# Optimization experiments

Hardware: AMD Instinct MI355X
Metric: run time of the kernel (lower is better)

The kernel has to match this reference:

```python
import jax, jax.numpy as jnp
import numpy as np

OUT, IN, GROUP, BITS = 8192, 8192, 128, 4
NG = IN // GROUP  # 64 groups per row

def unpack4(qweight):
    # qweight: [OUT, IN//2] uint8 -> [OUT, IN] int, low nibble first
    low = qweight & jnp.uint8(0x0F)
    high = qweight >> jnp.uint8(4)
    return jnp.stack([low, high], axis=-1).reshape(qweight.shape[0], -1)

def dequantize(qw, scale, zero):
    # qw: [OUT, IN] ints; scale/zero: [OUT, NG]
    q = qw.astype(scale.dtype).reshape(OUT, NG, GROUP)
    w = (q - zero[:, :, None]) * scale[:, :, None]
    return w.reshape(OUT, IN)

def setup_inputs() -> dict:
    key = jax.random.key(0)
    k1, k2, k3, k4 = jax.random.split(key, 4)
    x = jax.random.normal(k1, (8, IN), dtype=jnp.float32)
    qweight = jax.random.randint(k2, (OUT, IN // 2), 0, 256, dtype=jnp.int32).astype(jnp.uint8)
    scale = (jax.random.uniform(k3, (OUT, NG), dtype=jnp.float32) * 0.02 + 0.001)
    zero = jax.random.uniform(k4, (OUT, NG), dtype=jnp.float32) * 15.0
    return {"x": x, "qweight": qweight, "scale": scale, "zero": zero}

def reference(x, qweight, scale, zero):
    w = dequantize(unpack4(qweight), scale, zero)  # [OUT, IN]
    return x @ w.T  # F.linear(x, w), bias=None
```

## Files before the change

### kernel.cpp

```cpp
#include <hip/hip_runtime.h>


typedef __attribute__((ext_vector_type(8))) short bf16x8;
typedef __attribute__((ext_vector_type(4))) float f32x4;

constexpr int Mdim  = 8;
constexpr int N     = 8192;
constexpr int K     = 8192;
constexpr int NG    = 64;
constexpr int KS    = 16;
constexpr int KSL   = K / KS;
constexpr int GPS   = KSL / 128;
constexpr int ROWI4 = K / 8;
constexpr int SLKK  = KSL / 32;

__device__ __forceinline__ float nib_lo(int q) {
    return __int_as_float((q & 15) | 0x4B000000) - 8388608.0f;
}
__device__ __forceinline__ float nib_hi(int q) {
    return __int_as_float(((q >> 4) & 15) | 0x4B000000) - 8388608.0f;
}
__device__ __forceinline__ int pkbf(float lo, float hi) {
    int r;
    asm("v_cvt_pk_bf16_f32 %0, %1, %2" : "=v"(r) : "v"(lo), "v"(hi));
    return r;
}

__global__ __launch_bounds__(512, 4) void qmfma_kernel(
    const float* __restrict__ x,
    const int*   __restrict__ qw,
    const float* __restrict__ scale,
    const float* __restrict__ zero,
    float*       __restrict__ out)
{
    __shared__ int4 As[SLKK * 64];

    const int tid  = threadIdx.x;
    const int lane = tid & 63;
    const int wave = tid >> 6;
    const int bid  = blockIdx.x;
    const int ks   = bid >> 5;
    const int nb   = bid & 31;
    const int c0   = nb * 256 + wave * 32;
    const int nl0  = c0 + (lane & 15);
    const int nl1  = nl0 + 16;
    const int kb   = lane >> 4;

    const int4* __restrict__ qrow0 = reinterpret_cast<const int4*>(qw) + (size_t)nl0 * ROWI4;
    const int4* __restrict__ qrow1 = reinterpret_cast<const int4*>(qw) + (size_t)nl1 * ROWI4;

    const int g0 = ks * GPS;
    const int kq = ks * (KSL / 8);

    int4 qc0[4], qc1[4], qn0[4], qn1[4];
    #pragma unroll
    for (int t = 0; t < 4; ++t) {
        qc0[t] = qrow0[kq + t * 4 + kb];
        qc1[t] = qrow1[kq + t * 4 + kb];
    }
    float s0 = scale[nl0 * NG + g0], z0 = zero[nl0 * NG + g0];
    float s1 = scale[nl1 * NG + g0], z1 = zero[nl1 * NG + g0];

    #pragma unroll
    for (int j = tid; j < SLKK * 64; j += 512) {
        const int ll  = j & 63;
        const int kk  = j >> 6;
        const int row = ll & 15;
        const int k0  = ks * KSL + kk * 32 + (ll >> 4) * 8;
        float4 xa = {0.f, 0.f, 0.f, 0.f}, xb = {0.f, 0.f, 0.f, 0.f};
        if (row < Mdim) {
            const float4* xr = reinterpret_cast<const float4*>(x) + (size_t)row * (K / 4);
            xa = xr[k0 / 4];
            xb = xr[k0 / 4 + 1];
        }
        int4 r;
        r.x = pkbf(xa.x, xa.y);
        r.y = pkbf(xa.z, xa.w);
        r.z = pkbf(xb.x, xb.y);
        r.w = pkbf(xb.z, xb.w);
        As[j] = r;
    }
    __syncthreads();

    f32x4 acc0 = {0.f, 0.f, 0.f, 0.f};
    f32x4 acc1 = {0.f, 0.f, 0.f, 0.f};

    #pragma unroll 1
    for (int g = 0; g < GPS; ++g) {
        const float cs0 = s0, csz0 = z0 * s0;
        const float cs1 = s1, csz1 = z1 * s1;

        if (g + 1 < GPS) {
            const int kqn = kq + (g + 1) * 16;
            #pragma unroll
            for (int t = 0; t < 4; ++t) {
                qn0[t] = qrow0[kqn + t * 4 + kb];
                qn1[t] = qrow1[kqn + t * 4 + kb];
            }
            s0 = scale[nl0 * NG + g0 + g + 1]; z0 = zero[nl0 * NG + g0 + g + 1];
            s1 = scale[nl1 * NG + g0 + g + 1]; z1 = zero[nl1 * NG + g0 + g + 1];
        }

        #pragma unroll
        for (int t = 0; t < 4; ++t) {
            union { int4 u; bf16x8 v; } A;
            A.u = As[(g * 4 + t) * 64 + lane];

            union { int4 u; bf16x8 v; } B0, B1;
            const int4 qa = qc0[t];
            B0.u.x = pkbf(fmaf(nib_lo(qa.x), cs0, -csz0), fmaf(nib_hi(qa.x), cs0, -csz0));
            B0.u.y = pkbf(fmaf(nib_lo(qa.y), cs0, -csz0), fmaf(nib_hi(qa.y), cs0, -csz0));
            B0.u.z = pkbf(fmaf(nib_lo(qa.z), cs0, -csz0), fmaf(nib_hi(qa.z), cs0, -csz0));
            B0.u.w = pkbf(fmaf(nib_lo(qa.w), cs0, -csz0), fmaf(nib_hi(qa.w), cs0, -csz0));
            const int4 qb = qc1[t];
            B1.u.x = pkbf(fmaf(nib_lo(qb.x), cs1, -csz1), fmaf(nib_hi(qb.x), cs1, -csz1));
            B1.u.y = pkbf(fmaf(nib_lo(qb.y), cs1, -csz1), fmaf(nib_hi(qb.y), cs1, -csz1));
            B1.u.z = pkbf(fmaf(nib_lo(qb.z), cs1, -csz1), fmaf(nib_hi(qb.z), cs1, -csz1));
            B1.u.w = pkbf(fmaf(nib_lo(qb.w), cs1, -csz1), fmaf(nib_hi(qb.w), cs1, -csz1));

            acc0 = __builtin_amdgcn_mfma_f32_16x16x32_bf16(A.v, B0.v, acc0, 0, 0, 0);
            acc1 = __builtin_amdgcn_mfma_f32_16x16x32_bf16(A.v, B1.v, acc1, 0, 0, 0);
        }

        #pragma unroll
        for (int t = 0; t < 4; ++t) { qc0[t] = qn0[t]; qc1[t] = qn1[t]; }
    }

    if (kb < 2) {
        #pragma unroll
        for (int i = 0; i < 4; ++i) {
            const int m = kb * 4 + i;
            atomicAdd(&out[(size_t)m * N + nl0], acc0[i]);
            atomicAdd(&out[(size_t)m * N + nl1], acc1[i]);
        }
    }
}

extern "C" void kernel_launch(void* const* d_in, const int* in_sizes, int n_in,
                              void* d_out, int out_size, void* d_ws, size_t ws_size,
                              hipStream_t stream) {
    const float* x     = (const float*)d_in[0];
    const int*   qw    = (const int*)d_in[1];
    const float* scale = (const float*)d_in[2];
    const float* zero  = (const float*)d_in[3];
    float*       out   = (float*)d_out;

    hipMemsetAsync(out, 0, (size_t)Mdim * N * sizeof(float), stream);
    qmfma_kernel<<<(N / 256) * KS, 512, 0, stream>>>(x, qw, scale, zero, out);
}
```

Before: 42.67 us.

## Stage quantized weights through swizzled per-wave LDS for coalesced row loads

Quantized weight loads change so that each group of 16 lanes reads 256 contiguous bytes of a single weight row, instead of 16 lanes each reading a short 64-byte span from different rows. Each wave writes the loaded tiles into its own XOR-swizzled LDS buffer and reads them back in the MFMA B-operand layout. The next group's weights, scales and zeros are prefetched into registers and written to LDS after the current group's MFMAs. The aim is fuller global-memory transactions on this bandwidth-bound kernel. The cost is 64KB of extra LDS per block, which can lower occupancy, plus extra LDS traffic.

```diff
diff --git a/kernel.cpp b/kernel.cpp
--- a/kernel.cpp
+++ b/kernel.cpp
@@ -34,6 +34,7 @@
     float*       __restrict__ out)
 {
     __shared__ int4 As[SLKK * 64];
+    __shared__ int4 Bs[8][512];
 
     const int tid  = threadIdx.x;
     const int lane = tid & 63;
@@ -45,19 +46,20 @@
     const int nl0  = c0 + (lane & 15);
     const int nl1  = nl0 + 16;
     const int kb   = lane >> 4;
-
-    const int4* __restrict__ qrow0 = reinterpret_cast<const int4*>(qw) + (size_t)nl0 * ROWI4;
-    const int4* __restrict__ qrow1 = reinterpret_cast<const int4*>(qw) + (size_t)nl1 * ROWI4;
+    const int r    = lane & 15;
 
     const int g0 = ks * GPS;
     const int kq = ks * (KSL / 8);
 
-    int4 qc0[4], qc1[4], qn0[4], qn1[4];
+    const int4* __restrict__ qw4 = reinterpret_cast<const int4*>(qw);
+    const int4* __restrict__ bl  =
+        qw4 + (size_t)(c0 + (lane >> 4)) * ROWI4 + kq + (lane & 15);
+
+    int4 ln[8];
     #pragma unroll
-    for (int t = 0; t < 4; ++t) {
-        qc0[t] = qrow0[kq + t * 4 + kb];
-        qc1[t] = qrow1[kq + t * 4 + kb];
-    }
+    for (int i = 0; i < 8; ++i)
+        ln[i] = bl[(size_t)(4 * i) * ROWI4];
+
     float s0 = scale[nl0 * NG + g0], z0 = zero[nl0 * NG + g0];
     float s1 = scale[nl1 * NG + g0], z1 = zero[nl1 * NG + g0];
 
@@ -73,46 +75,51 @@
             xa = xr[k0 / 4];
             xb = xr[k0 / 4 + 1];
         }
-        int4 r;
-        r.x = pkbf(xa.x, xa.y);
-        r.y = pkbf(xa.z, xa.w);
-        r.z = pkbf(xb.x, xb.y);
-        r.w = pkbf(xb.z, xb.w);
-        As[j] = r;
+        int4 rr;
+        rr.x = pkbf(xa.x, xa.y);
+        rr.y = pkbf(xa.z, xa.w);
+        rr.z = pkbf(xb.x, xb.y);
+        rr.w = pkbf(xb.z, xb.w);
+        As[j] = rr;
+    }
+
+    #pragma unroll
+    for (int i = 0; i < 8; ++i) {
+        const int rl = 4 * i + (lane >> 4);
+        Bs[wave][rl * 16 + ((lane & 15) ^ (rl & 15))] = ln[i];
     }
     __syncthreads();
 
     f32x4 acc0 = {0.f, 0.f, 0.f, 0.f};
     f32x4 acc1 = {0.f, 0.f, 0.f, 0.f};
+    float s0n = 0.f, z0n = 0.f, s1n = 0.f, z1n = 0.f;
 
     #pragma unroll 1
     for (int g = 0; g < GPS; ++g) {
+        if (g + 1 < GPS) {
+            #pragma unroll
+            for (int i = 0; i < 8; ++i)
+                ln[i] = bl[(size_t)(4 * i) * ROWI4 + (g + 1) * 16];
+            s0n = scale[nl0 * NG + g0 + g + 1]; z0n = zero[nl0 * NG + g0 + g + 1];
+            s1n = scale[nl1 * NG + g0 + g + 1]; z1n = zero[nl1 * NG + g0 + g + 1];
+        }
+
         const float cs0 = s0, csz0 = z0 * s0;
         const float cs1 = s1, csz1 = z1 * s1;
 
-        if (g + 1 < GPS) {
-            const int kqn = kq + (g + 1) * 16;
-            #pragma unroll
-            for (int t = 0; t < 4; ++t) {
-                qn0[t] = qrow0[kqn + t * 4 + kb];
-                qn1[t] = qrow1[kqn + t * 4 + kb];
-            }
-            s0 = scale[nl0 * NG + g0 + g + 1]; z0 = zero[nl0 * NG + g0 + g + 1];
-            s1 = scale[nl1 * NG + g0 + g + 1]; z1 = zero[nl1 * NG + g0 + g + 1];
-        }
-
         #pragma unroll
         for (int t = 0; t < 4; ++t) {
-            union { int4 u; bf16x8 v; } A;
+            const int sl = (t * 4 + kb) ^ r;
+            const int4 qa = Bs[wave][r * 16 + sl];
+            const int4 qb = Bs[wave][(16 + r) * 16 + sl];
+
+            union { int4 u; bf16x8 v; } A, B0, B1;
             A.u = As[(g * 4 + t) * 64 + lane];
 
-            union { int4 u; bf16x8 v; } B0, B1;
-            const int4 qa = qc0[t];
             B0.u.x = pkbf(fmaf(nib_lo(qa.x), cs0, -csz0), fmaf(nib_hi(qa.x), cs0, -csz0));
             B0.u.y = pkbf(fmaf(nib_lo(qa.y), cs0, -csz0), fmaf(nib_hi(qa.y), cs0, -csz0));
             B0.u.z = pkbf(fmaf(nib_lo(qa.z), cs0, -csz0), fmaf(nib_hi(qa.z), cs0, -csz0));
             B0.u.w = pkbf(fmaf(nib_lo(qa.w), cs0, -csz0), fmaf(nib_hi(qa.w), cs0, -csz0));
-            const int4 qb = qc1[t];
             B1.u.x = pkbf(fmaf(nib_lo(qb.x), cs1, -csz1), fmaf(nib_hi(qb.x), cs1, -csz1));
             B1.u.y = pkbf(fmaf(nib_lo(qb.y), cs1, -csz1), fmaf(nib_hi(qb.y), cs1, -csz1));
             B1.u.z = pkbf(fmaf(nib_lo(qb.z), cs1, -csz1), fmaf(nib_hi(qb.z), cs1, -csz1));
@@ -122,8 +129,14 @@
             acc1 = __builtin_amdgcn_mfma_f32_16x16x32_bf16(A.v, B1.v, acc1, 0, 0, 0);
         }
 
-        #pragma unroll
-        for (int t = 0; t < 4; ++t) { qc0[t] = qn0[t]; qc1[t] = qn1[t]; }
+        if (g + 1 < GPS) {
+            #pragma unroll
+            for (int i = 0; i < 8; ++i) {
+                const int rl = 4 * i + (lane >> 4);
+                Bs[wave][rl * 16 + ((lane & 15) ^ (rl & 15))] = ln[i];
+            }
+            s0 = s0n; z0 = z0n; s1 = s1n; z1 = z1n;
+        }
     }
 
     if (kb < 2) {
```

New measurement: 70.08 us. 64.2% more time.
